# Performance work log

Measured on AMD Instinct MI355X. Metric: run time of the kernel, lower is better.

## Reference

```python
import jax, jax.numpy as jnp
import numpy as np

N_NODES = 50000


def _gcn_norm(edge_index, n):
    # PyG GCNConv default: add self-loops, symmetric normalization.
    src = jnp.concatenate([edge_index[0], jnp.arange(n, dtype=edge_index.dtype)])
    dst = jnp.concatenate([edge_index[1], jnp.arange(n, dtype=edge_index.dtype)])
    deg = jax.ops.segment_sum(jnp.ones_like(dst, dtype=jnp.float32), dst, num_segments=n)
    dinv = jnp.where(deg > 0, jax.lax.rsqrt(deg), 0.0)
    norm = dinv[src] * dinv[dst]  # [E+N]
    return src, dst, norm


def _gcn_conv(x, src, dst, norm, W, b):
    h = x @ W                                   # dense transform [N, out]
    msg = norm[:, None] * h[src]                # gather + scale  [E+N, out]
    out = jax.ops.segment_sum(msg, dst, num_segments=x.shape[0])  # scatter-add
    return out + b


def setup_inputs() -> dict:
    key = jax.random.key(0)
    k1, k2, k3, k4, k5 = jax.random.split(key, 5)
    d_in, d_hid, n_cls = 128, 128, 2
    x = jax.random.normal(k1, (N_NODES, d_in), dtype=jnp.float32)
    edge_index = jax.random.randint(k2, (2, 600000), 0, N_NODES, dtype=jnp.int64)
    # Glorot-ish scaled params
    W1 = jax.random.normal(k3, (d_in, d_hid), dtype=jnp.float32) / np.sqrt(d_in)
    b1 = jnp.zeros((d_hid,), dtype=jnp.float32)
    W2 = jax.random.normal(k4, (d_hid, n_cls), dtype=jnp.float32) / np.sqrt(d_hid)
    b2 = jnp.zeros((n_cls,), dtype=jnp.float32)
    return {"x": x, "edge_index": edge_index, "W1": W1, "b1": b1, "W2": W2, "b2": b2}


def reference(x, edge_index, W1, b1, W2, b2):
    n = x.shape[0]
    src, dst, norm = _gcn_norm(edge_index, n)
    h = _gcn_conv(x, src, dst, norm, W1, b1)
    h = jax.nn.relu(h)
    # dropout omitted (eval mode / deterministic reference)
    out = _gcn_conv(h, src, dst, norm, W2, b2)
    return out
```

## Files before the change

### kernel.cpp

```cpp
#include <hip/hip_runtime.h>
#include <stdint.h>


#define D 128
#define CAP 64
#define FILLB 512
#define GEMMB 782
#define NRT 3125

typedef short short8 __attribute__((ext_vector_type(8)));
typedef float f32x4 __attribute__((ext_vector_type(4)));

__device__ __forceinline__ float2 bf2_to_f2(unsigned int u) {
    float2 r;
    r.x = __uint_as_float(u << 16);
    r.y = __uint_as_float(u & 0xffff0000u);
    return r;
}
__device__ __forceinline__ unsigned short f2bf(float f) {
    unsigned int u = __float_as_uint(f);
    return (unsigned short)((u + 0x7fffu + ((u >> 16) & 1u)) >> 16);
}
__device__ __forceinline__ float bf2f(unsigned short s) {
    return __uint_as_float(((unsigned int)s) << 16);
}

__global__ __launch_bounds__(256) void zero_kernel(int4* __restrict__ p, int n4) {
    int i = blockIdx.x * 256 + threadIdx.x;
    if (i < n4) p[i] = make_int4(0, 0, 0, 0);
}

__global__ __launch_bounds__(256) void fill_gemm_kernel(
    const float* __restrict__ x, const int* __restrict__ ei,
    const float* __restrict__ W1,
    int* __restrict__ cnt, int* __restrict__ slots,
    unsigned short* __restrict__ h1u,
    int n, int E)
{
    const int tid = threadIdx.x;

    if (blockIdx.x < FILLB) {
        for (int e = blockIdx.x * 256 + tid; e < E; e += FILLB * 256) {
            int d = ei[E + e];
            int pos = atomicAdd(&cnt[d], 1);
            if (pos < CAP) slots[(size_t)d * CAP + pos] = ei[e];
        }
        return;
    }

    __shared__ unsigned short Ah[16 * 128];
    __shared__ unsigned short Al[16 * 128];

    const int wave = tid >> 6, lane = tid & 63;
    const int ln = lane & 15;
    const int kg = lane >> 4;
    const int cb = wave * 32;

    short8 bh[2][4], bl[2][4];
#pragma unroll
    for (int ct = 0; ct < 2; ++ct)
#pragma unroll
        for (int ks = 0; ks < 4; ++ks)
#pragma unroll
            for (int j = 0; j < 8; ++j) {
                float w = W1[(size_t)(ks * 32 + kg * 8 + j) * D + cb + ct * 16 + ln];
                unsigned short h = f2bf(w);
                bh[ct][ks][j] = (short)h;
                bl[ct][ks][j] = (short)f2bf(w - bf2f(h));
            }

    const int gb = blockIdx.x - FILLB;
    const int srow = tid >> 4;
    const int skb = (tid & 15) * 8;
    const int soff = ((srow * 128 + skb) ^ ((srow & 7) << 3));

    for (int it = 0; it < 4; ++it) {
        const int rt = gb * 4 + it;
        if (rt >= NRT) break;
        const int rowBase = rt * 16;

        {
            const float* xr = &x[(size_t)(rowBase + srow) * D + skb];
            float4 v0 = *(const float4*)xr;
            float4 v1 = *(const float4*)(xr + 4);
            const float f[8] = {v0.x, v0.y, v0.z, v0.w, v1.x, v1.y, v1.z, v1.w};
            short8 h8, l8;
#pragma unroll
            for (int j = 0; j < 8; ++j) {
                unsigned short h = f2bf(f[j]);
                h8[j] = (short)h;
                l8[j] = (short)f2bf(f[j] - bf2f(h));
            }
            *(short8*)&Ah[soff] = h8;
            *(short8*)&Al[soff] = l8;
        }
        __syncthreads();

        f32x4 acc[2];
#pragma unroll
        for (int ct = 0; ct < 2; ++ct) acc[ct] = (f32x4){0.f, 0.f, 0.f, 0.f};

#pragma unroll
        for (int ks = 0; ks < 4; ++ks) {
            const int aoff = ((ln * 128 + ks * 32 + kg * 8) ^ ((ln & 7) << 3));
            short8 ah = *(const short8*)&Ah[aoff];
            short8 al = *(const short8*)&Al[aoff];
#pragma unroll
            for (int ct = 0; ct < 2; ++ct) {
                acc[ct] = __builtin_amdgcn_mfma_f32_16x16x32_bf16(ah, bh[ct][ks], acc[ct], 0, 0, 0);
                acc[ct] = __builtin_amdgcn_mfma_f32_16x16x32_bf16(al, bh[ct][ks], acc[ct], 0, 0, 0);
                acc[ct] = __builtin_amdgcn_mfma_f32_16x16x32_bf16(ah, bl[ct][ks], acc[ct], 0, 0, 0);
            }
        }
        __syncthreads();

#pragma unroll
        for (int ct = 0; ct < 2; ++ct)
#pragma unroll
            for (int r = 0; r < 4; ++r) {
                int row = rowBase + kg * 4 + r;
                h1u[(size_t)row * D + cb + ct * 16 + ln] = f2bf(acc[ct][r]);
            }
    }
}

__global__ __launch_bounds__(256) void gather1_kernel(const int* __restrict__ cnt,
                                                      const int* __restrict__ slots,
                                                      const unsigned int* __restrict__ hs1b,
                                                      const float* __restrict__ b1,
                                                      const float* __restrict__ W2,
                                                      float* __restrict__ hs2, int n) {
    const int wave = threadIdx.x >> 6, lane = threadIdx.x & 63;
    const int i = blockIdx.x * 4 + wave;
    if (i >= n) return;

    const int ci = cnt[i];
    const int m = min(ci, CAP);
    const float di = rsqrtf((float)ci + 1.0f);
    int idx = (lane < m) ? slots[(size_t)i * CAP + lane] : 0;
    float dl = (lane < m) ? rsqrtf((float)cnt[idx] + 1.0f) : 0.f;

    float2 h = bf2_to_f2(hs1b[(size_t)i * 64 + lane]);
    float2 acc = make_float2(di * h.x, di * h.y);
    int j = 0;
    for (; j + 3 < m; j += 4) {
        int s0 = __shfl(idx, j, 64);
        int s1 = __shfl(idx, j + 1, 64);
        int s2 = __shfl(idx, j + 2, 64);
        int s3 = __shfl(idx, j + 3, 64);
        float d0 = __shfl(dl, j, 64);
        float d1 = __shfl(dl, j + 1, 64);
        float d2 = __shfl(dl, j + 2, 64);
        float d3 = __shfl(dl, j + 3, 64);
        float2 v0 = bf2_to_f2(hs1b[(size_t)s0 * 64 + lane]);
        float2 v1 = bf2_to_f2(hs1b[(size_t)s1 * 64 + lane]);
        float2 v2 = bf2_to_f2(hs1b[(size_t)s2 * 64 + lane]);
        float2 v3 = bf2_to_f2(hs1b[(size_t)s3 * 64 + lane]);
        acc.x = fmaf(d0, v0.x, fmaf(d1, v1.x, fmaf(d2, v2.x, fmaf(d3, v3.x, acc.x))));
        acc.y = fmaf(d0, v0.y, fmaf(d1, v1.y, fmaf(d2, v2.y, fmaf(d3, v3.y, acc.y))));
    }
    for (; j < m; ++j) {
        int s0 = __shfl(idx, j, 64);
        float d0 = __shfl(dl, j, 64);
        float2 v0 = bf2_to_f2(hs1b[(size_t)s0 * 64 + lane]);
        acc.x = fmaf(d0, v0.x, acc.x);
        acc.y = fmaf(d0, v0.y, acc.y);
    }

    float2 b = *(const float2*)&b1[lane * 2];
    float hx = fmaxf(fmaf(di, acc.x, b.x), 0.f);
    float hy = fmaxf(fmaf(di, acc.y, b.y), 0.f);

    float4 w = *(const float4*)&W2[lane * 4];
    float p0 = fmaf(hx, w.x, hy * w.z);
    float p1 = fmaf(hx, w.y, hy * w.w);
#pragma unroll
    for (int off = 32; off > 0; off >>= 1) {
        p0 += __shfl_xor(p0, off, 64);
        p1 += __shfl_xor(p1, off, 64);
    }
    if (lane == 0) {
        hs2[2 * i + 0] = di * p0;
        hs2[2 * i + 1] = di * p1;
    }
}

__global__ __launch_bounds__(256) void gather2_kernel(const int* __restrict__ cnt,
                                                      const int* __restrict__ slots,
                                                      const float* __restrict__ hs2,
                                                      const float* __restrict__ b2,
                                                      float* __restrict__ out, int n) {
    int i = blockIdx.x * 256 + threadIdx.x;
    if (i >= n) return;
    int m = min(cnt[i], CAP);
    float2 a = *(const float2*)&hs2[2 * i];
    const int* sl = &slots[(size_t)i * CAP];
    for (int e = 0; e < m; ++e) {
        int s = sl[e];
        float2 v = *(const float2*)&hs2[2 * s];
        a.x += v.x;
        a.y += v.y;
    }
    float di = rsqrtf((float)m + 1.0f);
    out[2 * i + 0] = fmaf(di, a.x, b2[0]);
    out[2 * i + 1] = fmaf(di, a.y, b2[1]);
}

extern "C" void kernel_launch(void* const* d_in, const int* in_sizes, int n_in,
                              void* d_out, int out_size, void* d_ws, size_t ws_size,
                              hipStream_t stream) {
    const float* x  = (const float*)d_in[0];
    const int*   ei = (const int*)d_in[1];
    const float* W1 = (const float*)d_in[2];
    const float* b1 = (const float*)d_in[3];
    const float* W2 = (const float*)d_in[4];
    const float* b2 = (const float*)d_in[5];

    const int n = in_sizes[0] / D;
    const int E = in_sizes[1] / 2;

    int* cnt           = (int*)d_ws;
    int* slots         = cnt + n;
    unsigned int* hs1b = (unsigned int*)(slots + (size_t)n * CAP);
    float* hs2         = (float*)(hs1b + (size_t)n * 64);
    float* out         = (float*)d_out;

    const int n4 = n / 4;

    zero_kernel<<<(n4 + 255) / 256, 256, 0, stream>>>((int4*)cnt, n4);
    fill_gemm_kernel<<<FILLB + GEMMB, 256, 0, stream>>>(
        x, ei, W1, cnt, slots, (unsigned short*)hs1b, n, E);
    gather1_kernel<<<(n + 3) / 4, 256, 0, stream>>>(cnt, slots, hs1b, b1, W2, hs2, n);
    gather2_kernel<<<(n + 255) / 256, 256, 0, stream>>>(cnt, slots, hs2, b2, out, n);
}
```

Before: 94.30 us.

## Split fused fill/GEMM kernel and software-pipeline x row-tile loads

Separates the combined edge-fill and dense-transform kernel into two launches: a one-thread-per-edge fill kernel and a GEMM kernel that handles more row tiles per block. The GEMM prefetches the next x tile into registers while the current tile's MFMAs run, and loads all W1 values before converting them to split-bf16. The aim is to hide global load latency and remove the grid-stride fill loop. In exchange it adds a kernel launch, drops the overlap of fill and GEMM within one launch, and uses fewer GEMM blocks, which lowers parallelism.

```diff
diff --git a/kernel.cpp b/kernel.cpp
--- a/kernel.cpp
+++ b/kernel.cpp
@@ -4,9 +4,8 @@
 
 #define D 128
 #define CAP 64
-#define FILLB 512
-#define GEMMB 782
 #define NRT 3125
+#define NT 8
 
 typedef short short8 __attribute__((ext_vector_type(8)));
 typedef float f32x4 __attribute__((ext_vector_type(4)));
@@ -30,32 +29,38 @@
     if (i < n4) p[i] = make_int4(0, 0, 0, 0);
 }
 
-__global__ __launch_bounds__(256) void fill_gemm_kernel(
-    const float* __restrict__ x, const int* __restrict__ ei,
-    const float* __restrict__ W1,
-    int* __restrict__ cnt, int* __restrict__ slots,
-    unsigned short* __restrict__ h1u,
-    int n, int E)
-{
-    const int tid = threadIdx.x;
-
-    if (blockIdx.x < FILLB) {
-        for (int e = blockIdx.x * 256 + tid; e < E; e += FILLB * 256) {
-            int d = ei[E + e];
-            int pos = atomicAdd(&cnt[d], 1);
-            if (pos < CAP) slots[(size_t)d * CAP + pos] = ei[e];
-        }
-        return;
-    }
-
+__global__ __launch_bounds__(256) void fill_kernel(const int* __restrict__ ei,
+                                                   int* __restrict__ cnt,
+                                                   int* __restrict__ slots, int E) {
+    int e = blockIdx.x * 256 + threadIdx.x;
+    if (e >= E) return;
+    int d = ei[E + e];
+    int pos = atomicAdd(&cnt[d], 1);
+    if (pos < CAP) slots[(size_t)d * CAP + pos] = ei[e];
+}
+
+__global__ __launch_bounds__(256) void gemm_kernel(const float* __restrict__ x,
+                                                   const float* __restrict__ W1,
+                                                   unsigned short* __restrict__ h1u,
+                                                   int n) {
     __shared__ unsigned short Ah[16 * 128];
     __shared__ unsigned short Al[16 * 128];
 
+    const int tid = threadIdx.x;
     const int wave = tid >> 6, lane = tid & 63;
     const int ln = lane & 15;
     const int kg = lane >> 4;
     const int cb = wave * 32;
 
+    float wv[2][4][8];
+#pragma unroll
+    for (int ct = 0; ct < 2; ++ct)
+#pragma unroll
+        for (int ks = 0; ks < 4; ++ks)
+#pragma unroll
+            for (int j = 0; j < 8; ++j)
+                wv[ct][ks][j] = W1[(size_t)(ks * 32 + kg * 8 + j) * D + cb + ct * 16 + ln];
+
     short8 bh[2][4], bl[2][4];
 #pragma unroll
     for (int ct = 0; ct < 2; ++ct)
@@ -63,27 +68,32 @@
         for (int ks = 0; ks < 4; ++ks)
 #pragma unroll
             for (int j = 0; j < 8; ++j) {
-                float w = W1[(size_t)(ks * 32 + kg * 8 + j) * D + cb + ct * 16 + ln];
+                float w = wv[ct][ks][j];
                 unsigned short h = f2bf(w);
                 bh[ct][ks][j] = (short)h;
                 bl[ct][ks][j] = (short)f2bf(w - bf2f(h));
             }
 
-    const int gb = blockIdx.x - FILLB;
+    const int rt0 = blockIdx.x * NT;
     const int srow = tid >> 4;
     const int skb = (tid & 15) * 8;
     const int soff = ((srow * 128 + skb) ^ ((srow & 7) << 3));
 
-    for (int it = 0; it < 4; ++it) {
-        const int rt = gb * 4 + it;
+    if (rt0 >= NRT) return;
+
+    float4 pv0, pv1;
+    {
+        const float* xr = &x[(size_t)(rt0 * 16 + srow) * D + skb];
+        pv0 = *(const float4*)xr;
+        pv1 = *(const float4*)(xr + 4);
+    }
+
+    for (int it = 0; it < NT; ++it) {
+        const int rt = rt0 + it;
         if (rt >= NRT) break;
-        const int rowBase = rt * 16;
 
         {
-            const float* xr = &x[(size_t)(rowBase + srow) * D + skb];
-            float4 v0 = *(const float4*)xr;
-            float4 v1 = *(const float4*)(xr + 4);
-            const float f[8] = {v0.x, v0.y, v0.z, v0.w, v1.x, v1.y, v1.z, v1.w};
+            const float f[8] = {pv0.x, pv0.y, pv0.z, pv0.w, pv1.x, pv1.y, pv1.z, pv1.w};
             short8 h8, l8;
 #pragma unroll
             for (int j = 0; j < 8; ++j) {
@@ -96,10 +106,15 @@
         }
         __syncthreads();
 
+        if (it + 1 < NT && rt + 1 < NRT) {
+            const float* xr = &x[(size_t)((rt + 1) * 16 + srow) * D + skb];
+            pv0 = *(const float4*)xr;
+            pv1 = *(const float4*)(xr + 4);
+        }
+
         f32x4 acc[2];
 #pragma unroll
         for (int ct = 0; ct < 2; ++ct) acc[ct] = (f32x4){0.f, 0.f, 0.f, 0.f};
-
 #pragma unroll
         for (int ks = 0; ks < 4; ++ks) {
             const int aoff = ((ln * 128 + ks * 32 + kg * 8) ^ ((ln & 7) << 3));
@@ -114,6 +129,7 @@
         }
         __syncthreads();
 
+        const int rowBase = rt * 16;
 #pragma unroll
         for (int ct = 0; ct < 2; ++ct)
 #pragma unroll
@@ -226,10 +242,11 @@
     float* out         = (float*)d_out;
 
     const int n4 = n / 4;
+    const int gemmB = (NRT + NT - 1) / NT;
 
     zero_kernel<<<(n4 + 255) / 256, 256, 0, stream>>>((int4*)cnt, n4);
-    fill_gemm_kernel<<<FILLB + GEMMB, 256, 0, stream>>>(
-        x, ei, W1, cnt, slots, (unsigned short*)hs1b, n, E);
+    fill_kernel<<<(E + 255) / 256, 256, 0, stream>>>(ei, cnt, slots, E);
+    gemm_kernel<<<gemmB, 256, 0, stream>>>(x, W1, (unsigned short*)hs1b, n);
     gather1_kernel<<<(n + 3) / 4, 256, 0, stream>>>(cnt, slots, hs1b, b1, W2, hs2, n);
     gather2_kernel<<<(n + 255) / 256, 256, 0, stream>>>(cnt, slots, hs2, b2, out, n);
 }
```

Measured after the change: 101.8 us. 7.9% more time.
